# Performance work log

Measured on AMD Instinct MI355X. Metric: run time of the kernel, lower is better.

## Reference

```python
import jax, jax.numpy as jnp
import numpy as np

DIM = 768

def setup_inputs() -> dict:
    key = jax.random.key(0)
    k1, k2, k3, k4, k5 = jax.random.split(key, 5)
    B, S, D = 16, 1024, DIM
    x = jax.random.normal(k1, (B, S, D), dtype=jnp.float32)
    # torch Linear weights: W has shape [out, in], y = x @ W.T + b
    w_qkv = jax.random.normal(k2, (3 * D, D), dtype=jnp.float32) * (D ** -0.5)
    b_qkv = jax.random.normal(k3, (3 * D,), dtype=jnp.float32) * 0.01
    w_out = jax.random.normal(k4, (D, D), dtype=jnp.float32) * (D ** -0.5)
    b_out = jax.random.normal(k5, (D,), dtype=jnp.float32) * 0.01
    return {"x": x, "w_qkv": w_qkv, "b_qkv": b_qkv, "w_out": w_out, "b_out": b_out}

def reference(x, w_qkv, b_qkv, w_out, b_out):
    D = x.shape[-1]
    qkv = jnp.einsum('bsd,ed->bse', x, w_qkv) + b_qkv  # [B,S,3D]
    q, k, v = jnp.split(qkv, 3, axis=-1)
    scale = D ** -0.5
    att = jnp.einsum('bqd,bkd->bqk', q, k) * scale  # [B,S,S]
    att = jax.nn.softmax(att, axis=-1)
    # dropout (p=0.1) is identity in eval mode
    out = jnp.einsum('bqk,bkd->bqd', att, v)
    return jnp.einsum('bsd,ed->bse', out, w_out) + b_out
```

## Files before the change

kernel.cpp:

```cpp
#include <hip/hip_runtime.h>
#include <hip/hip_bf16.h>
#include <math.h>

typedef __attribute__((ext_vector_type(8))) short bf16x8;
typedef __attribute__((ext_vector_type(4))) float f32x4;

__device__ __forceinline__ unsigned short f2bf_rne(float f) {
    union { float f; unsigned u; } x; x.f = f;
    unsigned r = x.u + 0x7FFFu + ((x.u >> 16) & 1u);
    return (unsigned short)(r >> 16);
}

__device__ __forceinline__ void store4(unsigned short* p, float v0, float v1, float v2, float v3) {
    ushort4 o; o.x = f2bf_rne(v0); o.y = f2bf_rne(v1); o.z = f2bf_rne(v2); o.w = f2bf_rne(v3);
    *(ushort4*)p = o;
}
__device__ __forceinline__ void store4(float* p, float v0, float v1, float v2, float v3) {
    float4 o; o.x = v0; o.y = v1; o.z = v2; o.w = v3;
    *(float4*)p = o;
}

__device__ __forceinline__ void async_copy16(const void* g, void* l) {
    __builtin_amdgcn_global_load_lds(
        (const __attribute__((address_space(1))) void*)g,
        (__attribute__((address_space(3))) void*)l, 16, 0, 0);
}

__global__ __launch_bounds__(256) void prep(
    const float* __restrict__ w_qkv, const float* __restrict__ b_qkv,
    const float* __restrict__ w_out, const float* __restrict__ b_out,
    unsigned short* __restrict__ wqT, unsigned short* __restrict__ wkT,
    unsigned short* __restrict__ wvT, unsigned short* __restrict__ wob,
    float* __restrict__ vpart, float* __restrict__ bpp, float* __restrict__ cbuf,
    float* __restrict__ rsum)
{
    const int blk = blockIdx.x;
    const int t   = threadIdx.x;
    if (blk < 432) {
        __shared__ float sh[64][65];
        __shared__ float pv[4][64];
        const int m  = blk / 144;
        const int r  = blk % 144;
        const int ty = r / 12;
        const int tx = r % 12;
        const float* W = w_qkv + (long long)m * 768 * 768;
        unsigned short* WT = (m == 0) ? wqT : (m == 1) ? wkT : wvT;
        const float* bsrc = (m == 0) ? (b_qkv + 768) : b_qkv;
        const int il = t & 63;
        const int ob = t >> 6;
        float acc = 0.f;
#pragma unroll
        for (int it = 0; it < 16; ++it) {
            const int ol = ob + it * 4;
            float w = W[(long long)(ty * 64 + ol) * 768 + tx * 64 + il];
            sh[ol][il] = w;
            if (m < 2) acc += w * bsrc[ty * 64 + ol];
        }
        __syncthreads();
#pragma unroll
        for (int it = 0; it < 16; ++it) {
            const int il2 = ob + it * 4;
            WT[(long long)(tx * 64 + il2) * 768 + ty * 64 + il] = f2bf_rne(sh[il][il2]);
        }
        if (m < 2) {
            pv[ob][il] = acc;
            __syncthreads();
            if (t < 64) {
                float s = pv[0][t] + pv[1][t] + pv[2][t] + pv[3][t];
                vpart[(m * 12 + ty) * 768 + tx * 64 + t] = s;
            }
        }
    } else if (blk < 624) {
        const int d = (blk - 432) * 4 + (t >> 6);
        const int l = t & 63;
        float s = 0.f;
        for (int o = l; o < 768; o += 64)
            s += w_out[(long long)d * 768 + o] * b_qkv[1536 + o];
        for (int off = 1; off < 64; off <<= 1) s += __shfl_xor(s, off);
        if (l == 0) bpp[d] = b_out[d] + s;
    } else if (blk == 624) {
        if (t < 64) {
            float s = 0.f;
            for (int o = t; o < 768; o += 64) s += b_qkv[o] * b_qkv[768 + o];
            for (int off = 1; off < 64; off <<= 1) s += __shfl_xor(s, off);
            if (t == 0) cbuf[0] = s;
        }
    } else if (blk < 1201) {
        const int j = (blk - 625) * 256 + t;
        float4 v = ((const float4*)w_out)[j];
        ushort4 o;
        o.x = f2bf_rne(v.x); o.y = f2bf_rne(v.y);
        o.z = f2bf_rne(v.z); o.w = f2bf_rne(v.w);
        ((ushort4*)wob)[j] = o;
    } else {
        const int j = (blk - 1201) * 256 + t;
        float4 z = {0.f, 0.f, 0.f, 0.f};
        ((float4*)rsum)[j] = z;
    }
}

__global__ __launch_bounds__(256) void finishv(
    const float* __restrict__ vpart, float* __restrict__ v1f, float* __restrict__ v2f)
{
    const int j = blockIdx.x * 256 + threadIdx.x;
    const int m = (j >= 768);
    const int i = j - m * 768;
    float s = 0.f;
#pragma unroll
    for (int ty = 0; ty < 12; ++ty) s += vpart[(m * 12 + ty) * 768 + i];
    (m ? v2f : v1f)[i] = s;
}

__global__ __launch_bounds__(256) void cvt_x(
    const float* __restrict__ x, unsigned short* __restrict__ xb,
    const float* __restrict__ v1f, const float* __restrict__ v2f,
    float* __restrict__ uf, float* __restrict__ wf)
{
    const int wave = threadIdx.x >> 6;
    const int lane = threadIdx.x & 63;
    const long long row = (long long)blockIdx.x * 4 + wave;
    const float4* xr = (const float4*)x + row * 192;
    ushort4* xbr = (ushort4*)xb + row * 192;
    const float4* v1 = (const float4*)v1f;
    const float4* v2 = (const float4*)v2f;
    float u = 0.f, w = 0.f;
#pragma unroll
    for (int j = 0; j < 3; ++j) {
        const int c = j * 64 + lane;
        float4 v = xr[c];
        ushort4 o;
        o.x = f2bf_rne(v.x); o.y = f2bf_rne(v.y);
        o.z = f2bf_rne(v.z); o.w = f2bf_rne(v.w);
        xbr[c] = o;
        float4 a = v1[c], b = v2[c];
        u += v.x * a.x + v.y * a.y + v.z * a.z + v.w * a.w;
        w += v.x * b.x + v.y * b.y + v.z * b.z + v.w * b.w;
    }
#pragma unroll
    for (int off = 1; off < 64; off <<= 1) {
        u += __shfl_xor(u, off);
        w += __shfl_xor(w, off);
    }
    if (lane == 0) { uf[row] = u; wf[row] = w; }
}

template <typename OutT, bool DO_EXP, bool DO_RSCALE, bool DO_VT>
__global__ __launch_bounds__(256) void gemm_nt_bf16(
    const unsigned short* __restrict__ A, int lda, long long strideA,
    const unsigned short* __restrict__ B, int ldb, long long strideB,
    OutT* __restrict__ C, int ldc, long long strideC,
    const float* __restrict__ bias, float scale, int K,
    float* __restrict__ rowsum, const float* __restrict__ rscale,
    unsigned short* __restrict__ vtp,
    const float* __restrict__ uf, const float* __restrict__ wf)
{
    __shared__ unsigned short shA[8448];
    __shared__ unsigned short shB[8448];

    const int t    = threadIdx.x;
    const int lane = t & 63;
    const int wave = t >> 6;
    const int wm   = (wave & 1) * 64;
    const int wn   = (wave >> 1) * 64;
    const int quad = lane >> 4;
    const int l16  = lane & 15;

    const int gx = gridDim.x, gy = gridDim.y;
    const int nwg = gx * gy * gridDim.z;
    const int orig = blockIdx.x + gx * (blockIdx.y + gy * blockIdx.z);
    const int id  = (orig & 7) * (nwg >> 3) + (orig >> 3);
    const int bx  = id % gx;
    const int rem = id / gx;
    const int by  = rem % gy;
    const int bz  = rem / gy;

    const long long batch = bz;
    A += batch * strideA;
    B += batch * strideB;
    C += batch * strideC;

    const long long tileM = (long long)by * 128;
    const long long tileN = (long long)bx * 128;
    const long long rowsPerBatch = (long long)gy * 128;

    f32x4 acc[4][4];
#pragma unroll
    for (int i = 0; i < 4; ++i)
#pragma unroll
        for (int j = 0; j < 4; ++j)
#pragma unroll
            for (int r = 0; r < 4; ++r) acc[i][j][r] = 0.0f;

    for (int k0 = 0; k0 < K; k0 += 64) {
        __syncthreads();
#pragma unroll
        for (int p = 0; p < 4; ++p) {
            const int g   = p * 256 + t;
            const int row = g >> 3;
            const int kg  = (g & 7) ^ (row & 7);
            async_copy16(A + (tileM + row) * (long long)lda + k0 + kg * 8, &shA[g << 3]);
            async_copy16(B + (tileN + row) * (long long)ldb + k0 + kg * 8, &shB[g << 3]);
        }
        __syncthreads();

#pragma unroll 1
        for (int h = 0; h < 2; ++h) {
            bf16x8 af[4], bfr[4];
#pragma unroll
            for (int mi = 0; mi < 4; ++mi) {
                const int row = wm + mi * 16 + l16;
                const int kg  = ((h << 2) | quad) ^ (row & 7);
                af[mi] = *(const bf16x8*)(&shA[row * 64 + kg * 8]);
            }
#pragma unroll
            for (int ni = 0; ni < 4; ++ni) {
                const int row = wn + ni * 16 + l16;
                const int kg  = ((h << 2) | quad) ^ (row & 7);
                bfr[ni] = *(const bf16x8*)(&shB[row * 64 + kg * 8]);
            }
#pragma unroll
            for (int mi = 0; mi < 4; ++mi)
#pragma unroll
                for (int ni = 0; ni < 4; ++ni)
                    acc[mi][ni] = __builtin_amdgcn_mfma_f32_16x16x32_bf16(
                        bfr[ni], af[mi], acc[mi][ni], 0, 0, 0);
        }
    }

    const bool vt_block = DO_VT && (tileN >= 768) && (tileN < 1536);
    if (vt_block) __syncthreads();
    unsigned short* const shd = (wn == 0) ? shA : shB;
    float cadd = 0.f;
    if (DO_EXP) cadd = rscale[0];
    const float* ufb = DO_EXP ? (uf + batch * rowsPerBatch) : nullptr;
    const float* wfb = DO_EXP ? (wf + batch * rowsPerBatch) : nullptr;
#pragma unroll
    for (int mi = 0; mi < 4; ++mi) {
        const long long gm = tileM + wm + mi * 16 + l16;
        float w = scale;
        if (DO_RSCALE) w = scale / rscale[batch * rowsPerBatch + gm];
        float uq = 0.f;
        if (DO_EXP) uq = ufb[gm] + cadd;
        float rsum = 0.0f;
#pragma unroll
        for (int ni = 0; ni < 4; ++ni) {
            const long long gn0 = tileN + wn + ni * 16 + quad * 4;
            float b0 = 0.f, b1 = 0.f, b2 = 0.f, b3 = 0.f;
            if (bias) {
                float4 bv = *(const float4*)&bias[gn0];
                b0 = bv.x; b1 = bv.y; b2 = bv.z; b3 = bv.w;
            }
            const f32x4 a = acc[mi][ni];
            float v0, v1, v2, v3;
            if (DO_EXP) {
                const float w0 = wfb[gn0 + 0];
                const float w1 = wfb[gn0 + 1];
                const float w2 = wfb[gn0 + 2];
                const float w3 = wfb[gn0 + 3];
                v0 = __expf((a[0] + uq + w0) * scale);
                v1 = __expf((a[1] + uq + w1) * scale);
                v2 = __expf((a[2] + uq + w2) * scale);
                v3 = __expf((a[3] + uq + w3) * scale);
                rsum += (v0 + v1) + (v2 + v3);
            } else {
                v0 = a[0] * w + b0; v1 = a[1] * w + b1;
                v2 = a[2] * w + b2; v3 = a[3] * w + b3;
            }
            if (vt_block) {
                const int dl = ni * 16 + quad * 4;
                const int kl = wm + mi * 16 + l16;
                shd[(dl + 0) * 132 + kl] = f2bf_rne(v0);
                shd[(dl + 1) * 132 + kl] = f2bf_rne(v1);
                shd[(dl + 2) * 132 + kl] = f2bf_rne(v2);
                shd[(dl + 3) * 132 + kl] = f2bf_rne(v3);
            } else {
                store4(C + gm * (long long)ldc + gn0, v0, v1, v2, v3);
            }
        }
        if (DO_EXP) {
            rsum += __shfl_xor(rsum, 16);
            rsum += __shfl_xor(rsum, 32);
            if (quad == 0)
                atomicAdd(&rowsum[batch * rowsPerBatch + gm], rsum);
        }
    }
    if (vt_block) {
        __syncthreads();
        const long long bvt  = tileM >> 10;
        const long long kin0 = tileM & 1023;
        const int dr = t >> 1;
        const int hf = t & 1;
        const unsigned short* src = (dr < 64) ? &shA[dr * 132] : &shB[(dr - 64) * 132];
        unsigned short* dst = vtp + (bvt * 768 + (tileN - 768) + dr) * 1024 + kin0 + hf * 64;
        src += hf * 64;
#pragma unroll
        for (int j = 0; j < 16; ++j)
            *(uint2*)(dst + j * 4) = *(const uint2*)(src + j * 4);
    }
}

extern "C" void kernel_launch(void* const* d_in, const int* in_sizes, int n_in,
                              void* d_out, int out_size, void* d_ws, size_t ws_size,
                              hipStream_t stream) {
    (void)in_sizes; (void)n_in; (void)out_size; (void)ws_size;

    const float* x     = (const float*)d_in[0];
    const float* w_qkv = (const float*)d_in[1];
    const float* b_qkv = (const float*)d_in[2];
    const float* w_out = (const float*)d_in[3];
    const float* b_out = (const float*)d_in[4];
    float* out = (float*)d_out;

    const int B = 16, S = 1024, D = 768;
    const long long MS = (long long)B * S;
    const int NB2 = 1536;

    unsigned short* xb  = (unsigned short*)d_ws;
    unsigned short* wob = xb  + MS * D;
    unsigned short* wqT = wob + (long long)D * D;
    unsigned short* wkT = wqT + (long long)D * D;
    unsigned short* wvT = wkT + (long long)D * D;
    unsigned short* B2  = wvT + (long long)D * D;
    unsigned short* xm  = B2  + (long long)NB2 * D;
    unsigned short* vwt = xm  + MS * NB2;
    unsigned short* att = vwt + (long long)B * D * S;
    float* rsum  = (float*)(att + (long long)B * S * S);
    float* v1f   = rsum + MS;
    float* v2f   = v1f + D;
    float* bpp   = v2f + D;
    float* cbuf  = bpp + D;
    float* uf    = cbuf + 4;
    float* wf    = uf + MS;
    float* vpart = wf + MS;

    prep<<<1217, 256, 0, stream>>>(w_qkv, b_qkv, w_out, b_out,
                                   wqT, wkT, wvT, wob, vpart, bpp, cbuf, rsum);

    finishv<<<6, 256, 0, stream>>>(vpart, v1f, v2f);

    gemm_nt_bf16<unsigned short, false, false, false><<<dim3(6, 6, 2), 256, 0, stream>>>(
        wkT, D, (long long)(wob - wkT),
        wqT, D, (long long)(wvT - wqT),
        B2,  D, (long long)D * D,
        nullptr, 1.0f, D, nullptr, nullptr, nullptr, nullptr, nullptr);

    cvt_x<<<4096, 256, 0, stream>>>(x, xb, v1f, v2f, uf, wf);

    gemm_nt_bf16<unsigned short, false, false, true><<<dim3(NB2 / 128, (int)(MS / 128), 1), 256, 0, stream>>>(
        xb, D, 0, B2, D, 0, xm, NB2, 0, nullptr, 1.0f, D, nullptr, nullptr, vwt, nullptr, nullptr);

    const float scale = 0.03608439182435162f;
    gemm_nt_bf16<unsigned short, true, false, false><<<dim3(S / 128, S / 128, B), 256, 0, stream>>>(
        xm, NB2, (long long)S * NB2,
        xb, D,   (long long)S * D,
        att, S,  (long long)S * S, nullptr, scale, D, rsum, cbuf, nullptr, uf, wf);

    gemm_nt_bf16<float, false, true, false><<<dim3(D / 128, S / 128, B), 256, 0, stream>>>(
        att, S, (long long)S * S,
        vwt, S, (long long)D * S,
        out, D, (long long)S * D, bpp, 1.0f, S, nullptr, rsum, nullptr, nullptr, nullptr);
}
```

Baseline: 274.1 us.

## Drop row-constant softmax terms and fuse weight GEMM with x conversion

Removes the query-row-constant terms (uf and the bq·bk constant) from the attention logits, because softmax is invariant to per-row additive shifts. This eliminates the v1 vector, the uf dot products and cbuf. Replaces the vpart/finishv reduction with atomicAdd into v2f, zeroed by a memset, and merges the small weight-product GEMM with the x-to-bf16 conversion into one launch, cutting launch count and serialization. The change trades a few small kernels for atomics and a heterogeneous fused kernel, and the exp now runs on unshifted logits whose magnitude differs.

Measured after the change: 259.8 us. 1.06x faster.

```diff
diff --git a/kernel.cpp b/kernel.cpp
--- a/kernel.cpp
+++ b/kernel.cpp
@@ -24,6 +24,50 @@
     __builtin_amdgcn_global_load_lds(
         (const __attribute__((address_space(1))) void*)g,
         (__attribute__((address_space(3))) void*)l, 16, 0, 0);
+}
+
+__device__ __forceinline__ void gemm_core128(
+    unsigned short* shA, unsigned short* shB,
+    const unsigned short* __restrict__ A, int lda,
+    const unsigned short* __restrict__ B, int ldb,
+    long long tileM, long long tileN, int K,
+    int t, int wm, int wn, int quad, int l16, f32x4 (&acc)[4][4])
+{
+    for (int k0 = 0; k0 < K; k0 += 64) {
+        __syncthreads();
+#pragma unroll
+        for (int p = 0; p < 4; ++p) {
+            const int g   = p * 256 + t;
+            const int row = g >> 3;
+            const int kg  = (g & 7) ^ (row & 7);
+            async_copy16(A + (tileM + row) * (long long)lda + k0 + kg * 8, &shA[g << 3]);
+            async_copy16(B + (tileN + row) * (long long)ldb + k0 + kg * 8, &shB[g << 3]);
+        }
+        __syncthreads();
+
+#pragma unroll 1
+        for (int h = 0; h < 2; ++h) {
+            bf16x8 af[4], bfr[4];
+#pragma unroll
+            for (int mi = 0; mi < 4; ++mi) {
+                const int row = wm + mi * 16 + l16;
+                const int kg  = ((h << 2) | quad) ^ (row & 7);
+                af[mi] = *(const bf16x8*)(&shA[row * 64 + kg * 8]);
+            }
+#pragma unroll
+            for (int ni = 0; ni < 4; ++ni) {
+                const int row = wn + ni * 16 + l16;
+                const int kg  = ((h << 2) | quad) ^ (row & 7);
+                bfr[ni] = *(const bf16x8*)(&shB[row * 64 + kg * 8]);
+            }
+#pragma unroll
+            for (int mi = 0; mi < 4; ++mi)
+#pragma unroll
+                for (int ni = 0; ni < 4; ++ni)
+                    acc[mi][ni] = __builtin_amdgcn_mfma_f32_16x16x32_bf16(
+                        bfr[ni], af[mi], acc[mi][ni], 0, 0, 0);
+        }
+    }
 }
 
 __global__ __launch_bounds__(256) void prep(
@@ -31,8 +75,7 @@
     const float* __restrict__ w_out, const float* __restrict__ b_out,
     unsigned short* __restrict__ wqT, unsigned short* __restrict__ wkT,
     unsigned short* __restrict__ wvT, unsigned short* __restrict__ wob,
-    float* __restrict__ vpart, float* __restrict__ bpp, float* __restrict__ cbuf,
-    float* __restrict__ rsum)
+    float* __restrict__ v2f, float* __restrict__ bpp)
 {
     const int blk = blockIdx.x;
     const int t   = threadIdx.x;
@@ -45,7 +88,6 @@
         const int tx = r % 12;
         const float* W = w_qkv + (long long)m * 768 * 768;
         unsigned short* WT = (m == 0) ? wqT : (m == 1) ? wkT : wvT;
-        const float* bsrc = (m == 0) ? (b_qkv + 768) : b_qkv;
         const int il = t & 63;
         const int ob = t >> 6;
         float acc = 0.f;
@@ -54,7 +96,7 @@
             const int ol = ob + it * 4;
             float w = W[(long long)(ty * 64 + ol) * 768 + tx * 64 + il];
             sh[ol][il] = w;
-            if (m < 2) acc += w * bsrc[ty * 64 + ol];
+            if (m == 1) acc += w * b_qkv[ty * 64 + ol];
         }
         __syncthreads();
 #pragma unroll
@@ -62,13 +104,11 @@
             const int il2 = ob + it * 4;
             WT[(long long)(tx * 64 + il2) * 768 + ty * 64 + il] = f2bf_rne(sh[il][il2]);
         }
-        if (m < 2) {
+        if (m == 1) {
             pv[ob][il] = acc;
             __syncthreads();
-            if (t < 64) {
-                float s = pv[0][t] + pv[1][t] + pv[2][t] + pv[3][t];
-                vpart[(m * 12 + ty) * 768 + tx * 64 + t] = s;
-            }
+            if (t < 64)
+                atomicAdd(&v2f[tx * 64 + t], pv[0][t] + pv[1][t] + pv[2][t] + pv[3][t]);
         }
     } else if (blk < 624) {
         const int d = (blk - 432) * 4 + (t >> 6);
@@ -78,70 +118,85 @@
             s += w_out[(long long)d * 768 + o] * b_qkv[1536 + o];
         for (int off = 1; off < 64; off <<= 1) s += __shfl_xor(s, off);
         if (l == 0) bpp[d] = b_out[d] + s;
-    } else if (blk == 624) {
-        if (t < 64) {
-            float s = 0.f;
-            for (int o = t; o < 768; o += 64) s += b_qkv[o] * b_qkv[768 + o];
-            for (int off = 1; off < 64; off <<= 1) s += __shfl_xor(s, off);
-            if (t == 0) cbuf[0] = s;
-        }
-    } else if (blk < 1201) {
-        const int j = (blk - 625) * 256 + t;
+    } else {
+        const int j = (blk - 624) * 256 + t;
         float4 v = ((const float4*)w_out)[j];
         ushort4 o;
         o.x = f2bf_rne(v.x); o.y = f2bf_rne(v.y);
         o.z = f2bf_rne(v.z); o.w = f2bf_rne(v.w);
         ((ushort4*)wob)[j] = o;
+    }
+}
+
+__global__ __launch_bounds__(256) void wgemm_cvt(
+    const unsigned short* __restrict__ wkT, const unsigned short* __restrict__ wqT,
+    const unsigned short* __restrict__ wob, const unsigned short* __restrict__ wvT,
+    unsigned short* __restrict__ B2,
+    const float* __restrict__ x, unsigned short* __restrict__ xb,
+    const float* __restrict__ v2f, float* __restrict__ wf)
+{
+    const int t = threadIdx.x;
+    if (blockIdx.x < 72) {
+        __shared__ unsigned short shA[8192];
+        __shared__ unsigned short shB[8192];
+        const int lane = t & 63;
+        const int wave = t >> 6;
+        const int wm   = (wave & 1) * 64;
+        const int wn   = (wave >> 1) * 64;
+        const int quad = lane >> 4;
+        const int l16  = lane & 15;
+        const int z  = blockIdx.x / 36;
+        const int r  = blockIdx.x % 36;
+        const long long tileM = (long long)(r / 6) * 128;
+        const long long tileN = (long long)(r % 6) * 128;
+        const unsigned short* A  = z ? wob : wkT;
+        const unsigned short* Bp = z ? wvT : wqT;
+        unsigned short* C = B2 + (long long)z * 768 * 768;
+
+        f32x4 acc[4][4];
+#pragma unroll
+        for (int i = 0; i < 4; ++i)
+#pragma unroll
+            for (int j = 0; j < 4; ++j)
+#pragma unroll
+                for (int rr = 0; rr < 4; ++rr) acc[i][j][rr] = 0.0f;
+
+        gemm_core128(shA, shB, A, 768, Bp, 768, tileM, tileN, 768,
+                     t, wm, wn, quad, l16, acc);
+
+#pragma unroll
+        for (int mi = 0; mi < 4; ++mi) {
+            const long long gm = tileM + wm + mi * 16 + l16;
+#pragma unroll
+            for (int ni = 0; ni < 4; ++ni) {
+                const long long gn0 = tileN + wn + ni * 16 + quad * 4;
+                const f32x4 a = acc[mi][ni];
+                store4(C + gm * 768 + gn0, a[0], a[1], a[2], a[3]);
+            }
+        }
     } else {
-        const int j = (blk - 1201) * 256 + t;
-        float4 z = {0.f, 0.f, 0.f, 0.f};
-        ((float4*)rsum)[j] = z;
-    }
-}
-
-__global__ __launch_bounds__(256) void finishv(
-    const float* __restrict__ vpart, float* __restrict__ v1f, float* __restrict__ v2f)
-{
-    const int j = blockIdx.x * 256 + threadIdx.x;
-    const int m = (j >= 768);
-    const int i = j - m * 768;
-    float s = 0.f;
-#pragma unroll
-    for (int ty = 0; ty < 12; ++ty) s += vpart[(m * 12 + ty) * 768 + i];
-    (m ? v2f : v1f)[i] = s;
-}
-
-__global__ __launch_bounds__(256) void cvt_x(
-    const float* __restrict__ x, unsigned short* __restrict__ xb,
-    const float* __restrict__ v1f, const float* __restrict__ v2f,
-    float* __restrict__ uf, float* __restrict__ wf)
-{
-    const int wave = threadIdx.x >> 6;
-    const int lane = threadIdx.x & 63;
-    const long long row = (long long)blockIdx.x * 4 + wave;
-    const float4* xr = (const float4*)x + row * 192;
-    ushort4* xbr = (ushort4*)xb + row * 192;
-    const float4* v1 = (const float4*)v1f;
-    const float4* v2 = (const float4*)v2f;
-    float u = 0.f, w = 0.f;
-#pragma unroll
-    for (int j = 0; j < 3; ++j) {
-        const int c = j * 64 + lane;
-        float4 v = xr[c];
-        ushort4 o;
-        o.x = f2bf_rne(v.x); o.y = f2bf_rne(v.y);
-        o.z = f2bf_rne(v.z); o.w = f2bf_rne(v.w);
-        xbr[c] = o;
-        float4 a = v1[c], b = v2[c];
-        u += v.x * a.x + v.y * a.y + v.z * a.z + v.w * a.w;
-        w += v.x * b.x + v.y * b.y + v.z * b.z + v.w * b.w;
-    }
-#pragma unroll
-    for (int off = 1; off < 64; off <<= 1) {
-        u += __shfl_xor(u, off);
-        w += __shfl_xor(w, off);
-    }
-    if (lane == 0) { uf[row] = u; wf[row] = w; }
+        const int wave = t >> 6;
+        const int lane = t & 63;
+        const long long row = (long long)(blockIdx.x - 72) * 4 + wave;
+        const float4* xr = (const float4*)x + row * 192;
+        ushort4* xbr = (ushort4*)xb + row * 192;
+        const float4* v2 = (const float4*)v2f;
+        float w = 0.f;
+#pragma unroll
+        for (int j = 0; j < 3; ++j) {
+            const int c = j * 64 + lane;
+            float4 v = xr[c];
+            ushort4 o;
+            o.x = f2bf_rne(v.x); o.y = f2bf_rne(v.y);
+            o.z = f2bf_rne(v.z); o.w = f2bf_rne(v.w);
+            xbr[c] = o;
+            float4 b = v2[c];
+            w += v.x * b.x + v.y * b.y + v.z * b.z + v.w * b.w;
+        }
+#pragma unroll
+        for (int off = 1; off < 64; off <<= 1) w += __shfl_xor(w, off);
+        if (lane == 0) wf[row] = w;
+    }
 }
 
 template <typename OutT, bool DO_EXP, bool DO_RSCALE, bool DO_VT>
@@ -151,8 +206,7 @@
     OutT* __restrict__ C, int ldc, long long strideC,
     const float* __restrict__ bias, float scale, int K,
     float* __restrict__ rowsum, const float* __restrict__ rscale,
-    unsigned short* __restrict__ vtp,
-    const float* __restrict__ uf, const float* __restrict__ wf)
+    unsigned short* __restrict__ vtp, const float* __restrict__ wf)
 {
     __shared__ unsigned short shA[8448];
     __shared__ unsigned short shB[8448];
@@ -191,56 +245,27 @@
 #pragma unroll
             for (int r = 0; r < 4; ++r) acc[i][j][r] = 0.0f;
 
-    for (int k0 = 0; k0 < K; k0 += 64) {
-        __syncthreads();
-#pragma unroll
-        for (int p = 0; p < 4; ++p) {
-            const int g   = p * 256 + t;
-            const int row = g >> 3;
-            const int kg  = (g & 7) ^ (row & 7);
-            async_copy16(A + (tileM + row) * (long long)lda + k0 + kg * 8, &shA[g << 3]);
-            async_copy16(B + (tileN + row) * (long long)ldb + k0 + kg * 8, &shB[g << 3]);
-        }
-        __syncthreads();
-
-#pragma unroll 1
-        for (int h = 0; h < 2; ++h) {
-            bf16x8 af[4], bfr[4];
-#pragma unroll
-            for (int mi = 0; mi < 4; ++mi) {
-                const int row = wm + mi * 16 + l16;
-                const int kg  = ((h << 2) | quad) ^ (row & 7);
-                af[mi] = *(const bf16x8*)(&shA[row * 64 + kg * 8]);
-            }
-#pragma unroll
-            for (int ni = 0; ni < 4; ++ni) {
-                const int row = wn + ni * 16 + l16;
-                const int kg  = ((h << 2) | quad) ^ (row & 7);
-                bfr[ni] = *(const bf16x8*)(&shB[row * 64 + kg * 8]);
-            }
-#pragma unroll
-            for (int mi = 0; mi < 4; ++mi)
-#pragma unroll
-                for (int ni = 0; ni < 4; ++ni)
-                    acc[mi][ni] = __builtin_amdgcn_mfma_f32_16x16x32_bf16(
-                        bfr[ni], af[mi], acc[mi][ni], 0, 0, 0);
-        }
-    }
+    gemm_core128(shA, shB, A, lda, B, ldb, tileM, tileN, K, t, wm, wn, quad, l16, acc);
 
     const bool vt_block = DO_VT && (tileN >= 768) && (tileN < 1536);
     if (vt_block) __syncthreads();
     unsigned short* const shd = (wn == 0) ? shA : shB;
-    float cadd = 0.f;
-    if (DO_EXP) cadd = rscale[0];
-    const float* ufb = DO_EXP ? (uf + batch * rowsPerBatch) : nullptr;
-    const float* wfb = DO_EXP ? (wf + batch * rowsPerBatch) : nullptr;
+
+    float wkv[4][4];
+    if (DO_EXP) {
+        const float* wfb = wf + batch * rowsPerBatch;
+#pragma unroll
+        for (int ni = 0; ni < 4; ++ni) {
+            const long long gn0 = tileN + wn + ni * 16 + quad * 4;
+            float4 t4 = *(const float4*)&wfb[gn0];
+            wkv[ni][0] = t4.x; wkv[ni][1] = t4.y; wkv[ni][2] = t4.z; wkv[ni][3] = t4.w;
+        }
+    }
 #pragma unroll
     for (int mi = 0; mi < 4; ++mi) {
         const long long gm = tileM + wm + mi * 16 + l16;
         float w = scale;
         if (DO_RSCALE) w = scale / rscale[batch * rowsPerBatch + gm];
-        float uq = 0.f;
-        if (DO_EXP) uq = ufb[gm] + cadd;
         float rsum = 0.0f;
 #pragma unroll
         for (int ni = 0; ni < 4; ++ni) {
@@ -253,14 +278,10 @@
             const f32x4 a = acc[mi][ni];
             float v0, v1, v2, v3;
             if (DO_EXP) {
-                const float w0 = wfb[gn0 + 0];
-                const float w1 = wfb[gn0 + 1];
-                const float w2 = wfb[gn0 + 2];
-                const float w3 = wfb[gn0 + 3];
-                v0 = __expf((a[0] + uq + w0) * scale);
-                v1 = __expf((a[1] + uq + w1) * scale);
-                v2 = __expf((a[2] + uq + w2) * scale);
-                v3 = __expf((a[3] + uq + w3) * scale);
+                v0 = __expf((a[0] + wkv[ni][0]) * scale);
+                v1 = __expf((a[1] + wkv[ni][1]) * scale);
+                v2 = __expf((a[2] + wkv[ni][2]) * scale);
+                v3 = __expf((a[3] + wkv[ni][3]) * scale);
                 rsum += (v0 + v1) + (v2 + v3);
             } else {
                 v0 = a[0] * w + b0; v1 = a[1] * w + b1;
@@ -324,39 +345,29 @@
     unsigned short* xm  = B2  + (long long)NB2 * D;
     unsigned short* vwt = xm  + MS * NB2;
     unsigned short* att = vwt + (long long)B * D * S;
-    float* rsum  = (float*)(att + (long long)B * S * S);
-    float* v1f   = rsum + MS;
-    float* v2f   = v1f + D;
-    float* bpp   = v2f + D;
-    float* cbuf  = bpp + D;
-    float* uf    = cbuf + 4;
-    float* wf    = uf + MS;
-    float* vpart = wf + MS;
-
-    prep<<<1217, 256, 0, stream>>>(w_qkv, b_qkv, w_out, b_out,
-                                   wqT, wkT, wvT, wob, vpart, bpp, cbuf, rsum);
-
-    finishv<<<6, 256, 0, stream>>>(vpart, v1f, v2f);
-
-    gemm_nt_bf16<unsigned short, false, false, false><<<dim3(6, 6, 2), 256, 0, stream>>>(
-        wkT, D, (long long)(wob - wkT),
-        wqT, D, (long long)(wvT - wqT),
-        B2,  D, (long long)D * D,
-        nullptr, 1.0f, D, nullptr, nullptr, nullptr, nullptr, nullptr);
-
-    cvt_x<<<4096, 256, 0, stream>>>(x, xb, v1f, v2f, uf, wf);
+    float* rsum = (float*)(att + (long long)B * S * S);
+    float* v2f  = rsum + MS;
+    float* bpp  = v2f + D;
+    float* wf   = bpp + D;
+
+    hipMemsetAsync(rsum, 0, (size_t)(MS + D) * sizeof(float), stream);
+
+    prep<<<1200, 256, 0, stream>>>(w_qkv, b_qkv, w_out, b_out,
+                                   wqT, wkT, wvT, wob, v2f, bpp);
+
+    wgemm_cvt<<<4168, 256, 0, stream>>>(wkT, wqT, wob, wvT, B2, x, xb, v2f, wf);
 
     gemm_nt_bf16<unsigned short, false, false, true><<<dim3(NB2 / 128, (int)(MS / 128), 1), 256, 0, stream>>>(
-        xb, D, 0, B2, D, 0, xm, NB2, 0, nullptr, 1.0f, D, nullptr, nullptr, vwt, nullptr, nullptr);
+        xb, D, 0, B2, D, 0, xm, NB2, 0, nullptr, 1.0f, D, nullptr, nullptr, vwt, nullptr);
 
     const float scale = 0.03608439182435162f;
     gemm_nt_bf16<unsigned short, true, false, false><<<dim3(S / 128, S / 128, B), 256, 0, stream>>>(
         xm, NB2, (long long)S * NB2,
         xb, D,   (long long)S * D,
-        att, S,  (long long)S * S, nullptr, scale, D, rsum, cbuf, nullptr, uf, wf);
+        att, S,  (long long)S * S, nullptr, scale, D, rsum, nullptr, nullptr, wf);
 
     gemm_nt_bf16<float, false, true, false><<<dim3(D / 128, S / 128, B), 256, 0, stream>>>(
         att, S, (long long)S * S,
         vwt, S, (long long)D * S,
-        out, D, (long long)S * D, bpp, 1.0f, S, nullptr, rsum, nullptr, nullptr, nullptr);
-}
+        out, D, (long long)S * D, bpp, 1.0f, S, nullptr, rsum, nullptr, nullptr);
+}
```
